# Kernel tuning notes

Measured on AMD Instinct MI355X. Metric: run time of the kernel, lower is better.

Reference implementation:

```python
import jax, jax.numpy as jnp
import numpy as np

NUM_HEADS = 8
WINDOW = (2, 8, 8)
NW = 64  # number of distinct window masks
TOPK = 2  # selected_n + 1


def _rel_position_index(ws):
    d, h, w = ws
    coords = np.stack(np.meshgrid(np.arange(d), np.arange(h), np.arange(w), indexing='ij'))  # (3,d,h,w)
    flat = coords.reshape(3, -1)  # (3,N)
    rel = flat[:, :, None] - flat[:, None, :]  # (3,N,N)
    rel = rel.transpose(1, 2, 0).astype(np.int64)
    rel[..., 0] += d - 1
    rel[..., 1] += h - 1
    rel[..., 2] += w - 1
    rel[..., 0] *= (2 * h - 1) * (2 * w - 1)
    rel[..., 1] *= 2 * w - 1
    return jnp.asarray(rel.sum(-1), dtype=jnp.int32)  # (N,N)


def setup_inputs() -> dict:
    key = jax.random.key(0)
    ks = jax.random.split(key, 7)
    B_, N, C = 1024, 128, 128
    x = jax.random.normal(ks[0], (B_, N, C), jnp.float32)
    mask = jax.random.normal(ks[1], (NW, N, N), jnp.float32)
    Wq = jax.random.normal(ks[2], (C, C), jnp.float32) * 0.02
    Wkv = jax.random.normal(ks[3], (C, 2 * C), jnp.float32) * 0.02
    Wproj = jax.random.normal(ks[4], (C, C), jnp.float32) * 0.02
    bproj = jnp.zeros((C,), jnp.float32)
    tbl_len = (2 * WINDOW[0] - 1) * (2 * WINDOW[1] - 1) * (2 * WINDOW[2] - 1)  # 675
    bias_table = jax.random.normal(ks[5], (tbl_len, NUM_HEADS), jnp.float32) * 0.02
    rel_index = _rel_position_index(WINDOW)
    return dict(x=x, mask=mask, Wq=Wq, Wkv=Wkv, Wproj=Wproj, bproj=bproj,
                bias_table=bias_table, rel_index=rel_index)


def reference(x, mask, Wq, Wkv, Wproj, bproj, bias_table, rel_index):
    B_, N, C = x.shape
    h = NUM_HEADS
    hd = C // h
    scale = hd ** -0.5
    # q/k/v projections (qkv_bias=False)
    q = (x @ Wq).reshape(B_, N, h, hd).transpose(0, 2, 1, 3)            # (B_,h,N,hd)
    kv = (x @ Wkv).reshape(B_, N, 2, h, hd).transpose(2, 0, 3, 1, 4)    # (2,B_,h,N,hd)
    k, v = kv[0], kv[1]
    attn = jnp.einsum('bhnd,bhmd->bhnm', q * scale, k)                  # (B_,h,N,N)
    # gathered relative-position bias
    bias = bias_table[rel_index.reshape(-1)].reshape(N, N, h).transpose(2, 0, 1)
    attn = attn + bias[None]
    nW = mask.shape[0]
    attn = attn.reshape(B_ // nW, nW, h, N, N) + mask[None, :, None]
    attn = jax.nn.softmax(attn.reshape(B_, h, N, N), axis=-1)
    # only_one branch: top-k gather + weighted sum over V
    sv, si = jax.lax.top_k(attn, TOPK)                                  # (B_,h,N,K)
    sel = jnp.take_along_axis(v, si.reshape(B_, h, N * TOPK)[..., None], axis=2)
    sel = sel.reshape(B_, h, N, TOPK, hd)
    out = (sel * sv[..., None]).sum(axis=3)                             # (B_,h,N,hd)
    xo = out.transpose(0, 2, 1, 3).reshape(B_, N, C)
    return xo @ Wproj + bproj
```

## Files before the change

kernel.cpp:

```cpp
#include <hip/hip_runtime.h>
#include <hip/hip_bf16.h>
#include <stdint.h>

typedef __attribute__((ext_vector_type(8))) short short8;
typedef __attribute__((ext_vector_type(4))) float floatx4;

#define B_TOT 1024
#define N_TOK 128
#define C_DIM 128
#define NHEAD 8
#define NW_MASK 64

#define BIAS_OFF 0
#define WALL_OFF 524288
#define WHEAD_BYTES 30464
#define WPT_OFF 768000
#define WS_BYTES 800768

#define QS_LDS 0
#define KS_LDS 14336
#define VS_LDS 43008
#define XO_LDS 60416
#define WB_LDS 70656
#define WPTB_LDS 132096
#define LDS_BYTES 148480

#define MFMA(a, b, c) __builtin_amdgcn_mfma_f32_16x16x32_bf16((a), (b), (c), 0, 0, 0)

__device__ __forceinline__ float bf2f(ushort u) {
  union { uint32_t u; float f; } v; v.u = ((uint32_t)u) << 16; return v.f;
}
__device__ __forceinline__ ushort f2bf(float f) {
  uint32_t u = __float_as_uint(f);
  return (ushort)((u + 0x7FFFu + ((u >> 16) & 1u)) >> 16);
}
__device__ __forceinline__ void split3(float f, ushort& h, ushort& m, ushort& l) {
  h = f2bf(f);  float r  = f - bf2f(h);
  m = f2bf(r);  float r2 = r - bf2f(m);
  l = f2bf(r2);
}
__device__ __forceinline__ void split3t(float f, ushort& h, ushort& m, ushort& l) {
  h = (ushort)(__float_as_uint(f) >> 16);
  float r  = f - bf2f(h);
  m = (ushort)(__float_as_uint(r) >> 16);
  float r2 = r - bf2f(m);
  l = f2bf(r2);
}

__device__ __forceinline__ void dma16(const void* g, void* l_) {
  __builtin_amdgcn_global_load_lds((const __attribute__((address_space(1))) void*)g,
                                   (__attribute__((address_space(3))) void*)l_,
                                   16, 0, 0);
}

__global__ __launch_bounds__(512)
void prep_kernel(const int* __restrict__ rel_index, const float* __restrict__ table,
                 const float* __restrict__ Wq, const float* __restrict__ Wkv,
                 const float* __restrict__ Wproj, char* __restrict__ ws) {
  float*  bias_g = (float*)(ws + BIAS_OFF);
  ushort* wpt_g  = (ushort*)(ws + WPT_OFF);

  int idx = blockIdx.x * 512 + threadIdx.x;
  if (idx < 131072) {
    int h = idx >> 14, mn = idx & 16383;
    bias_g[idx] = table[rel_index[mn] * NHEAD + h];
  } else if (idx < 131072 + 16384) {
    int t = idx - 131072;
    int h = t >> 11, r = t & 2047, oc = r >> 7, kk = r & 127;
    ushort a, bb, cc;
    split3(Wq[kk * C_DIM + h * 16 + oc] * 0.25f, a, bb, cc);
    ushort* wqp = (ushort*)(ws + WALL_OFF + h * WHEAD_BYTES);
    wqp[0 * 2176 + oc * 136 + kk] = a;
    wqp[1 * 2176 + oc * 136 + kk] = bb;
    wqp[2 * 2176 + oc * 136 + kk] = cc;
  } else if (idx < 131072 + 2 * 16384) {
    int t = idx - 131072 - 16384;
    int h = t >> 11, r = t & 2047, oc = r >> 7, kk = r & 127;
    ushort a, bb, cc;
    split3(Wkv[kk * (2 * C_DIM) + h * 16 + oc], a, bb, cc);
    ushort* wkp = (ushort*)(ws + WALL_OFF + h * WHEAD_BYTES) + 6528;
    wkp[0 * 2176 + oc * 136 + kk] = a;
    wkp[1 * 2176 + oc * 136 + kk] = bb;
    wkp[2 * 2176 + oc * 136 + kk] = cc;
  } else if (idx < 131072 + 3 * 16384) {
    int t = idx - 131072 - 2 * 16384;
    int h = t >> 11, r = t & 2047, oc = r >> 7, kk = r & 127;
    ushort* wvp = (ushort*)(ws + WALL_OFF + h * WHEAD_BYTES) + 13056;
    wvp[oc * 136 + kk] = f2bf(Wkv[kk * (2 * C_DIM) + C_DIM + h * 16 + oc]);
  } else if (idx < 131072 + 4 * 16384) {
    int t = idx - 131072 - 3 * 16384;
    int hp = t >> 12, r = t & 4095, n = r >> 5, kk = r & 31;
    wpt_g[t] = f2bf(Wproj[(hp * 32 + kk) * C_DIM + n]);
  }
}

__global__ __launch_bounds__(512, 2)
void wattn_kernel(const float* __restrict__ x, const float* __restrict__ mask,
                  const float* __restrict__ bproj, const char* __restrict__ ws,
                  float* __restrict__ out) {
  extern __shared__ char smem[];
  ushort* qs = (ushort*)(smem + QS_LDS);
  ushort* xo = (ushort*)(smem + XO_LDS);

  const float* bias_g = (const float*)(ws + BIAS_OFF);

  const int tid  = threadIdx.x;
  const int w    = tid >> 6;
  const int l    = tid & 63;
  const int quad = l >> 4;
  const int c    = l & 15;
  const int b    = blockIdx.x;
  const int wi   = b & (NW_MASK - 1);

  {
    const char* src = ws + WALL_OFF;
    char* dst = smem + WB_LDS;
    #pragma unroll
    for (int t = 0; t < 4; ++t) {
      int ch = t * 8 + w;
      if (ch < 30) dma16(src + ch * 1024 + l * 16, dst + ch * 1024 + l * 16);
    }
    dma16(ws + WPT_OFF + w * 1024 + l * 16, smem + WPTB_LDS + w * 1024 + l * 16);
  }

  short8 A1[8], A3[8];
  {
    const float* xrow = x + ((size_t)b * N_TOK + 16 * w + c) * C_DIM;
    #pragma unroll
    for (int kt = 0; kt < 8; ++kt) {
      int colb = kt * 16 + (quad & 1) * 8;
      floatx4 xa  = *(const floatx4*)(xrow + colb);
      floatx4 xb2 = *(const floatx4*)(xrow + colb + 4);
      short8 hi8, mi8, lo8;
      #pragma unroll
      for (int jj = 0; jj < 8; ++jj) {
        float f = (jj < 4) ? xa[jj] : xb2[jj - 4];
        ushort hh, mm, ll; split3t(f, hh, mm, ll);
        hi8[jj] = (short)hh; mi8[jj] = (short)mm; lo8[jj] = (short)ll;
      }
      A1[kt] = (quad < 2) ? hi8 : mi8;
      A3[kt] = (quad < 2) ? hi8 : lo8;
    }
  }

  floatx4 oacc[8];
  #pragma unroll
  for (int j = 0; j < 8; ++j) oacc[j] = (floatx4){0.f, 0.f, 0.f, 0.f};

  asm volatile("s_waitcnt vmcnt(0)" ::: "memory");
  __syncthreads();

  for (int h = 0; h < NHEAD; ++h) {
    ushort* ks_c = (ushort*)(smem + KS_LDS + (h & 1) * 14336);
    float*  vs_c = (float*)(smem + VS_LDS + (h & 1) * 8704);

    if (h < 7) {
      const char* src = ws + WALL_OFF + (h + 1) * WHEAD_BYTES;
      char* dst = smem + WB_LDS + ((h + 1) & 1) * 30720;
      #pragma unroll
      for (int t = 0; t < 4; ++t) {
        int ch = t * 8 + w;
        if (ch < 30) dma16(src + ch * 1024 + l * 16, dst + ch * 1024 + l * 16);
      }
      if (h & 1) {
        int np = (h + 1) >> 1;
        dma16(ws + WPT_OFF + np * 8192 + w * 1024 + l * 16,
              smem + WPTB_LDS + (np & 1) * 8192 + w * 1024 + l * 16);
      }
    }

    {
      floatx4 aq = (floatx4){0.f,0.f,0.f,0.f};
      floatx4 ak = (floatx4){0.f,0.f,0.f,0.f};
      floatx4 av = (floatx4){0.f,0.f,0.f,0.f};
      const ushort* wh  = (const ushort*)(smem + WB_LDS + (h & 1) * 30720);
      const ushort* wqp = wh + c * 136;
      const ushort* wkp = wh + 6528 + c * 136;
      const ushort* wvp = wh + 13056 + c * 136;
      const int q3off = (quad < 2) ? 2 * 2176 : 0;
      #pragma unroll
      for (int kt = 0; kt < 8; ++kt) {
        int colb = kt * 16 + (quad & 1) * 8;
        short8 bq1 = *(const short8*)(wqp + colb);
        short8 bq2 = *(const short8*)(wqp + 2176 + colb);
        short8 bq3 = *(const short8*)(wqp + q3off + colb);
        aq = MFMA(A1[kt], bq1, aq);  aq = MFMA(A1[kt], bq2, aq);  aq = MFMA(A3[kt], bq3, aq);
        short8 bk1 = *(const short8*)(wkp + colb);
        short8 bk2 = *(const short8*)(wkp + 2176 + colb);
        short8 bk3 = *(const short8*)(wkp + q3off + colb);
        ak = MFMA(A1[kt], bk1, ak);  ak = MFMA(A1[kt], bk2, ak);  ak = MFMA(A3[kt], bk3, ak);
        short8 bv1 = *(const short8*)(wvp + colb);
        av = MFMA(A1[kt], bv1, av);
      }
      #pragma unroll
      for (int i = 0; i < 4; ++i) {
        int tok = 16 * w + 4 * quad + i;
        ushort a, bb, cc;
        split3t(aq[i], a, bb, cc);
        qs[tok * 56 + c] = a; qs[tok * 56 + 16 + c] = bb; qs[tok * 56 + 32 + c] = cc;
        split3t(ak[i], a, bb, cc);
        ks_c[tok * 56 + c] = a; ks_c[tok * 56 + 16 + c] = bb; ks_c[tok * 56 + 32 + c] = cc;
        vs_c[tok * 17 + c] = av[i];
      }
    }
    __syncthreads();

    {
      const ushort* qrow = qs + (16 * w + c) * 56;
      short8 aq1 = *(const short8*)(qrow + quad * 8);
      short8 aq3 = *(const short8*)(qrow + ((quad < 2) ? quad * 8 : 16 + quad * 8));

      float m1[4], m2[4], psum[4];
      int   i1[4], i2[4];
      #pragma unroll
      for (int i = 0; i < 4; ++i) {
        m1[i] = -__builtin_inff(); i1[i] = 0;
        m2[i] = -__builtin_inff(); i2[i] = -1;
        psum[i] = 0.0f;
      }

      #pragma unroll
      for (int j = 0; j < 8; ++j) {
        floatx4 acc = (floatx4){0.f, 0.f, 0.f, 0.f};
        const ushort* krow = ks_c + (16 * j + c) * 56;
        int bo1 = (quad & 1) * 8;
        short8 b1 = *(const short8*)(krow + bo1);
        short8 b2 = *(const short8*)(krow + 16 + bo1);
        short8 b3 = *(const short8*)(krow + ((quad < 2) ? 32 + quad * 8
                                                        : (quad - 2) * 8));
        acc = MFMA(aq1, b1, acc);
        acc = MFMA(aq1, b2, acc);
        acc = MFMA(aq3, b3, acc);

        #pragma unroll
        for (int i = 0; i < 4; ++i) {
          int m = 16 * w + 4 * quad + i;
          int n = 16 * j + c;
          float v = acc[i] + bias_g[(h * N_TOK + m) * N_TOK + n] +
                             mask[(wi * N_TOK + m) * N_TOK + n];
          psum[i] += __expf(v);
          int col = 16 * j + c;
          bool g1 = v > m1[i];
          bool g2 = (!g1) && (v > m2[i]);
          m2[i] = g1 ? m1[i] : (g2 ? v : m2[i]);
          i2[i] = g1 ? i1[i] : (g2 ? col : i2[i]);
          m1[i] = g1 ? v : m1[i];
          i1[i] = g1 ? col : i1[i];
        }
      }

      #pragma unroll
      for (int i = 0; i < 4; ++i) {
        float M1 = m1[i], M2 = m2[i], PS = psum[i];
        int I1 = i1[i], I2 = i2[i];
        #pragma unroll
        for (int d = 1; d < 16; d <<= 1) {
          float om1 = __shfl_xor(M1, d); int oi1 = __shfl_xor(I1, d);
          float om2 = __shfl_xor(M2, d); int oi2 = __shfl_xor(I2, d);
          float ops = __shfl_xor(PS, d);
          bool aw = (M1 > om1) || (M1 == om1 && I1 < oi1);
          float lv = aw ? om1 : M1;  int li = aw ? oi1 : I1;
          float sv = aw ? M2 : om2;  int si = aw ? I2 : oi2;
          M1 = aw ? M1 : om1;  I1 = aw ? I1 : oi1;
          bool sb = (sv > lv) || (sv == lv && si < li);
          M2 = sb ? sv : lv; I2 = sb ? si : li;
          PS += ops;
        }
        float inv = 1.0f / PS;
        float p1 = __expf(M1) * inv;
        float p2 = __expf(M2) * inv;
        int tok = 16 * w + 4 * quad + i;
        float o = p1 * vs_c[I1 * 17 + c] + p2 * vs_c[I2 * 17 + c];
        xo[tok * 40 + (h & 1) * 16 + c] = f2bf(o);
      }
    }

    if (h & 1) {
      const ushort* wptp = (const ushort*)(smem + WPTB_LDS + ((h >> 1) & 1) * 8192);
      short8 a = *(const short8*)(xo + (16 * w + c) * 40 + quad * 8);
      #pragma unroll
      for (int j = 0; j < 8; ++j) {
        short8 bf = *(const short8*)(wptp + (16 * j + c) * 32 + quad * 8);
        oacc[j] = MFMA(a, bf, oacc[j]);
      }
    }
  }

  #pragma unroll
  for (int j = 0; j < 8; ++j) {
    float bp = bproj[16 * j + c];
    #pragma unroll
    for (int i = 0; i < 4; ++i) {
      int row = 16 * w + 4 * quad + i;
      out[((size_t)b * N_TOK + row) * C_DIM + 16 * j + c] = oacc[j][i] + bp;
    }
  }
}

extern "C" void kernel_launch(void* const* d_in, const int* in_sizes, int n_in,
                              void* d_out, int out_size, void* d_ws, size_t ws_size,
                              hipStream_t stream) {
  const float* x     = (const float*)d_in[0];
  const float* mask  = (const float*)d_in[1];
  const float* Wq    = (const float*)d_in[2];
  const float* Wkv   = (const float*)d_in[3];
  const float* Wproj = (const float*)d_in[4];
  const float* bproj = (const float*)d_in[5];
  const float* btab  = (const float*)d_in[6];
  const int*   ridx  = (const int*)d_in[7];
  float* outp = (float*)d_out;
  char*  ws   = (char*)d_ws;

  (void)in_sizes; (void)n_in; (void)out_size; (void)ws_size;

  hipFuncSetAttribute(reinterpret_cast<const void*>(wattn_kernel),
                      hipFuncAttributeMaxDynamicSharedMemorySize, LDS_BYTES);

  prep_kernel<<<384, 512, 0, stream>>>(ridx, btab, Wq, Wkv, Wproj, ws);
  wattn_kernel<<<B_TOT, 512, LDS_BYTES, stream>>>(x, mask, bproj, ws, outp);
}
```

Measured before the change: 381.6 us.

## Shrink LDS footprint by single-buffering weights and storing Q as fp32

```diff
diff --git a/kernel.cpp b/kernel.cpp
--- a/kernel.cpp
+++ b/kernel.cpp
@@ -3,7 +3,9 @@
 #include <stdint.h>
 
 typedef __attribute__((ext_vector_type(8))) short short8;
+typedef __attribute__((ext_vector_type(4))) short short4v;
 typedef __attribute__((ext_vector_type(4))) float floatx4;
+typedef __attribute__((ext_vector_type(2))) float floatx2;
 
 #define B_TOT 1024
 #define N_TOK 128
@@ -13,17 +15,17 @@
 
 #define BIAS_OFF 0
 #define WALL_OFF 524288
-#define WHEAD_BYTES 30464
-#define WPT_OFF 768000
-#define WS_BYTES 800768
+#define WHEAD_SLOT 30720
+#define WPT_OFF 770048
+#define WS_BYTES 806912
 
 #define QS_LDS 0
-#define KS_LDS 14336
-#define VS_LDS 43008
-#define XO_LDS 60416
-#define WB_LDS 70656
-#define WPTB_LDS 132096
-#define LDS_BYTES 148480
+#define KS_LDS 9216
+#define VS_LDS 23552
+#define XO_LDS 31744
+#define WB_LDS 40960
+#define WPT_LDS 71680
+#define LDS_BYTES 80896
 
 #define MFMA(a, b, c) __builtin_amdgcn_mfma_f32_16x16x32_bf16((a), (b), (c), 0, 0, 0)
 
@@ -69,7 +71,7 @@
     int h = t >> 11, r = t & 2047, oc = r >> 7, kk = r & 127;
     ushort a, bb, cc;
     split3(Wq[kk * C_DIM + h * 16 + oc] * 0.25f, a, bb, cc);
-    ushort* wqp = (ushort*)(ws + WALL_OFF + h * WHEAD_BYTES);
+    ushort* wqp = (ushort*)(ws + WALL_OFF + h * WHEAD_SLOT);
     wqp[0 * 2176 + oc * 136 + kk] = a;
     wqp[1 * 2176 + oc * 136 + kk] = bb;
     wqp[2 * 2176 + oc * 136 + kk] = cc;
@@ -78,29 +80,31 @@
     int h = t >> 11, r = t & 2047, oc = r >> 7, kk = r & 127;
     ushort a, bb, cc;
     split3(Wkv[kk * (2 * C_DIM) + h * 16 + oc], a, bb, cc);
-    ushort* wkp = (ushort*)(ws + WALL_OFF + h * WHEAD_BYTES) + 6528;
+    ushort* wkp = (ushort*)(ws + WALL_OFF + h * WHEAD_SLOT) + 6528;
     wkp[0 * 2176 + oc * 136 + kk] = a;
     wkp[1 * 2176 + oc * 136 + kk] = bb;
     wkp[2 * 2176 + oc * 136 + kk] = cc;
   } else if (idx < 131072 + 3 * 16384) {
     int t = idx - 131072 - 2 * 16384;
     int h = t >> 11, r = t & 2047, oc = r >> 7, kk = r & 127;
-    ushort* wvp = (ushort*)(ws + WALL_OFF + h * WHEAD_BYTES) + 13056;
+    ushort* wvp = (ushort*)(ws + WALL_OFF + h * WHEAD_SLOT) + 13056;
     wvp[oc * 136 + kk] = f2bf(Wkv[kk * (2 * C_DIM) + C_DIM + h * 16 + oc]);
   } else if (idx < 131072 + 4 * 16384) {
     int t = idx - 131072 - 3 * 16384;
     int hp = t >> 12, r = t & 4095, n = r >> 5, kk = r & 31;
-    wpt_g[t] = f2bf(Wproj[(hp * 32 + kk) * C_DIM + n]);
-  }
-}
-
-__global__ __launch_bounds__(512, 2)
+    wpt_g[hp * 4608 + n * 36 + kk] = f2bf(Wproj[(hp * 32 + kk) * C_DIM + n]);
+  }
+}
+
+__global__ __launch_bounds__(512, 4)
 void wattn_kernel(const float* __restrict__ x, const float* __restrict__ mask,
                   const float* __restrict__ bproj, const char* __restrict__ ws,
                   float* __restrict__ out) {
   extern __shared__ char smem[];
-  ushort* qs = (ushort*)(smem + QS_LDS);
-  ushort* xo = (ushort*)(smem + XO_LDS);
+  float*  qs_f = (float*)(smem + QS_LDS);
+  ushort* ks   = (ushort*)(smem + KS_LDS);
+  float*  vs   = (float*)(smem + VS_LDS);
+  ushort* xo   = (ushort*)(smem + XO_LDS);
 
   const float* bias_g = (const float*)(ws + BIAS_OFF);
 
@@ -120,7 +124,12 @@
       int ch = t * 8 + w;
       if (ch < 30) dma16(src + ch * 1024 + l * 16, dst + ch * 1024 + l * 16);
     }
-    dma16(ws + WPT_OFF + w * 1024 + l * 16, smem + WPTB_LDS + w * 1024 + l * 16);
+    #pragma unroll
+    for (int t = 0; t < 2; ++t) {
+      int ch = t * 8 + w;
+      if (ch < 9) dma16(ws + WPT_OFF + ch * 1024 + l * 16,
+                        smem + WPT_LDS + ch * 1024 + l * 16);
+    }
   }
 
   short8 A1[8], A3[8];
@@ -151,29 +160,11 @@
   __syncthreads();
 
   for (int h = 0; h < NHEAD; ++h) {
-    ushort* ks_c = (ushort*)(smem + KS_LDS + (h & 1) * 14336);
-    float*  vs_c = (float*)(smem + VS_LDS + (h & 1) * 8704);
-
-    if (h < 7) {
-      const char* src = ws + WALL_OFF + (h + 1) * WHEAD_BYTES;
-      char* dst = smem + WB_LDS + ((h + 1) & 1) * 30720;
-      #pragma unroll
-      for (int t = 0; t < 4; ++t) {
-        int ch = t * 8 + w;
-        if (ch < 30) dma16(src + ch * 1024 + l * 16, dst + ch * 1024 + l * 16);
-      }
-      if (h & 1) {
-        int np = (h + 1) >> 1;
-        dma16(ws + WPT_OFF + np * 8192 + w * 1024 + l * 16,
-              smem + WPTB_LDS + (np & 1) * 8192 + w * 1024 + l * 16);
-      }
-    }
-
     {
       floatx4 aq = (floatx4){0.f,0.f,0.f,0.f};
       floatx4 ak = (floatx4){0.f,0.f,0.f,0.f};
       floatx4 av = (floatx4){0.f,0.f,0.f,0.f};
-      const ushort* wh  = (const ushort*)(smem + WB_LDS + (h & 1) * 30720);
+      const ushort* wh  = (const ushort*)(smem + WB_LDS);
       const ushort* wqp = wh + c * 136;
       const ushort* wkp = wh + 6528 + c * 136;
       const ushort* wvp = wh + 13056 + c * 136;
@@ -195,20 +186,49 @@
       #pragma unroll
       for (int i = 0; i < 4; ++i) {
         int tok = 16 * w + 4 * quad + i;
+        qs_f[tok * 18 + c] = aq[i];
         ushort a, bb, cc;
-        split3t(aq[i], a, bb, cc);
-        qs[tok * 56 + c] = a; qs[tok * 56 + 16 + c] = bb; qs[tok * 56 + 32 + c] = cc;
         split3t(ak[i], a, bb, cc);
-        ks_c[tok * 56 + c] = a; ks_c[tok * 56 + 16 + c] = bb; ks_c[tok * 56 + 32 + c] = cc;
-        vs_c[tok * 17 + c] = av[i];
+        ks[tok * 56 + c] = a; ks[tok * 56 + 16 + c] = bb; ks[tok * 56 + 32 + c] = cc;
+        vs[tok * 16 + c] = av[i];
       }
     }
     __syncthreads();
 
+    if (h < 7) {
+      const char* src = ws + WALL_OFF + (h + 1) * WHEAD_SLOT;
+      char* dst = smem + WB_LDS;
+      #pragma unroll
+      for (int t = 0; t < 4; ++t) {
+        int ch = t * 8 + w;
+        if (ch < 30) dma16(src + ch * 1024 + l * 16, dst + ch * 1024 + l * 16);
+      }
+    }
+    if (h >= 2 && !(h & 1)) {
+      int p = h >> 1;
+      #pragma unroll
+      for (int t = 0; t < 2; ++t) {
+        int ch = t * 8 + w;
+        if (ch < 9) dma16(ws + WPT_OFF + p * 9216 + ch * 1024 + l * 16,
+                          smem + WPT_LDS + ch * 1024 + l * 16);
+      }
+    }
+
     {
-      const ushort* qrow = qs + (16 * w + c) * 56;
-      short8 aq1 = *(const short8*)(qrow + quad * 8);
-      short8 aq3 = *(const short8*)(qrow + ((quad < 2) ? quad * 8 : 16 + quad * 8));
+      short8 aq1, aq3;
+      {
+        const float* qrowf = qs_f + (16 * w + c) * 18 + (quad & 1) * 8;
+        floatx2 qf[4];
+        #pragma unroll
+        for (int p = 0; p < 4; ++p) qf[p] = *(const floatx2*)(qrowf + 2 * p);
+        #pragma unroll
+        for (int jj = 0; jj < 8; ++jj) {
+          float f = qf[jj >> 1][jj & 1];
+          ushort hh, mm, ll; split3t(f, hh, mm, ll);
+          aq1[jj] = (short)((quad < 2) ? hh : mm);
+          aq3[jj] = (short)((quad < 2) ? hh : ll);
+        }
+      }
 
       float m1[4], m2[4], psum[4];
       int   i1[4], i2[4];
@@ -222,7 +242,7 @@
       #pragma unroll
       for (int j = 0; j < 8; ++j) {
         floatx4 acc = (floatx4){0.f, 0.f, 0.f, 0.f};
-        const ushort* krow = ks_c + (16 * j + c) * 56;
+        const ushort* krow = ks + (16 * j + c) * 56;
         int bo1 = (quad & 1) * 8;
         short8 b1 = *(const short8*)(krow + bo1);
         short8 b2 = *(const short8*)(krow + 16 + bo1);
@@ -270,20 +290,28 @@
         float p1 = __expf(M1) * inv;
         float p2 = __expf(M2) * inv;
         int tok = 16 * w + 4 * quad + i;
-        float o = p1 * vs_c[I1 * 17 + c] + p2 * vs_c[I2 * 17 + c];
-        xo[tok * 40 + (h & 1) * 16 + c] = f2bf(o);
+        float o = p1 * vs[I1 * 16 + c] + p2 * vs[I2 * 16 + c];
+        xo[tok * 36 + (h & 1) * 16 + c] = f2bf(o);
       }
     }
 
     if (h & 1) {
-      const ushort* wptp = (const ushort*)(smem + WPTB_LDS + ((h >> 1) & 1) * 8192);
-      short8 a = *(const short8*)(xo + (16 * w + c) * 40 + quad * 8);
+      const ushort* wpt_l = (const ushort*)(smem + WPT_LDS);
+      int row = 16 * w + c;
+      short4v alo = *(const short4v*)(xo + row * 36 + quad * 8);
+      short4v ahi = *(const short4v*)(xo + row * 36 + quad * 8 + 4);
+      short8 a = __builtin_shufflevector(alo, ahi, 0, 1, 2, 3, 4, 5, 6, 7);
       #pragma unroll
       for (int j = 0; j < 8; ++j) {
-        short8 bf = *(const short8*)(wptp + (16 * j + c) * 32 + quad * 8);
+        const ushort* wr = wpt_l + (16 * j + c) * 36 + quad * 8;
+        short4v blo = *(const short4v*)(wr);
+        short4v bhi = *(const short4v*)(wr + 4);
+        short8 bf = __builtin_shufflevector(blo, bhi, 0, 1, 2, 3, 4, 5, 6, 7);
         oacc[j] = MFMA(a, bf, oacc[j]);
       }
     }
+
+    if (h < 7) __syncthreads();
   }
 
   #pragma unroll
```

Measured after the change: 827.4 us. 2.17x slower.
